# Performance work log

Measured on AMD Instinct MI355X. Metric: run time of the kernel, lower is better.

Reference implementation:

```python
import jax, jax.numpy as jnp
import numpy as np

B, T, D = 8, 1024, 256
H, KD = 8, 256          # keras MHA built with key_dim=embed_dim -> per-head dim = D
FF = 1024
WIN = 64                # causal sliding window size
G = 2                   # num_global_tokens (last-k tokens of the sequence)
EPS = 1e-6
NEG = -1e9


def _mha(q_in, kv_in, Wq, bq, Wk, bk, Wv, bv, Wo, bo, mask=None):
    """Keras-style MultiHeadAttention. q_in:[B,Tq,D], kv_in:[B,Ts,D] -> [B,Tq,D]."""
    q = jnp.einsum('btd,dhk->bthk', q_in, Wq) + bq
    k = jnp.einsum('bsd,dhk->bshk', kv_in, Wk) + bk
    v = jnp.einsum('bsd,dhk->bshk', kv_in, Wv) + bv
    s = jnp.einsum('bthk,bshk->bhts', q, k) / jnp.sqrt(jnp.asarray(KD, q.dtype))
    if mask is not None:
        s = jnp.where(mask, s, jnp.asarray(NEG, s.dtype))
    a = jax.nn.softmax(s, axis=-1)
    o = jnp.einsum('bhts,bshk->bthk', a, v)
    return jnp.einsum('bthk,hkd->btd', o, Wo) + bo


def _ln(x, g, b):
    m = jnp.mean(x, axis=-1, keepdims=True)
    v = jnp.mean(jnp.square(x - m), axis=-1, keepdims=True)
    return (x - m) * jax.lax.rsqrt(v + EPS) * g + b


def setup_inputs() -> dict:
    key = jax.random.key(0)
    ks = jax.random.split(key, 32)
    sp = 1.0 / np.sqrt(D)   # proj fan-in D
    so = 1.0 / np.sqrt(H * KD)

    def mha_params(k0):
        k = jax.random.split(k0, 4)
        return dict(
            Wq=jax.random.normal(k[0], (D, H, KD), jnp.float32) * sp,
            Wk=jax.random.normal(k[1], (D, H, KD), jnp.float32) * sp,
            Wv=jax.random.normal(k[2], (D, H, KD), jnp.float32) * sp,
            Wo=jax.random.normal(k[3], (H, KD, D), jnp.float32) * so,
        )
    lp = mha_params(ks[1])
    gp = mha_params(ks[2])
    inp = {
        'x': jax.random.normal(ks[0], (B, T, D), jnp.float32),
        'lWq': lp['Wq'], 'lbq': jnp.zeros((H, KD), jnp.float32),
        'lWk': lp['Wk'], 'lbk': jnp.zeros((H, KD), jnp.float32),
        'lWv': lp['Wv'], 'lbv': jnp.zeros((H, KD), jnp.float32),
        'lWo': lp['Wo'], 'lbo': jnp.zeros((D,), jnp.float32),
        'gWq': gp['Wq'], 'gbq': jnp.zeros((H, KD), jnp.float32),
        'gWk': gp['Wk'], 'gbk': jnp.zeros((H, KD), jnp.float32),
        'gWv': gp['Wv'], 'gbv': jnp.zeros((H, KD), jnp.float32),
        'gWo': gp['Wo'], 'gbo': jnp.zeros((D,), jnp.float32),
        'fW1': jax.random.normal(ks[3], (D, FF), jnp.float32) * sp,
        'fb1': jnp.zeros((FF,), jnp.float32),
        'fW2': jax.random.normal(ks[4], (FF, D), jnp.float32) * (1.0 / np.sqrt(FF)),
        'fb2': jnp.zeros((D,), jnp.float32),
        'ln1_g': jnp.ones((D,), jnp.float32), 'ln1_b': jnp.zeros((D,), jnp.float32),
        'ln2_g': jnp.ones((D,), jnp.float32), 'ln2_b': jnp.zeros((D,), jnp.float32),
    }
    return inp


def reference(x, lWq, lbq, lWk, lbk, lWv, lbv, lWo, lbo,
              gWq, gbq, gWk, gbk, gWv, gbv, gWo, gbo,
              fW1, fb1, fW2, fb2, ln1_g, ln1_b, ln2_g, ln2_b):
    i = jnp.arange(T)[:, None]
    j = jnp.arange(T)[None, :]
    win_mask = (j <= i) & (j > i - WIN)            # [T,T]
    win_mask = win_mask[None, None]                # [1,1,T,T]

    # Local window attention (the original per-timestep loop, fused via mask).
    local = _mha(x, x, lWq, lbq, lWk, lbk, lWv, lbv, lWo, lbo, mask=win_mask)

    # Global tokens: last G tokens attend to full sequence, then tokens attend to them.
    g = x[:, T - G:, :]                            # [B,G,D]
    g2 = _mha(g, x, gWq, gbq, gWk, gbk, gWv, gbv, gWo, gbo)
    gx = _mha(x, g2, gWq, gbq, gWk, gbk, gWv, gbv, gWo, gbo)

    attn_out = local + gx
    out1 = _ln(x + attn_out, ln1_g, ln1_b)
    ffn = jnp.maximum(out1 @ fW1 + fb1, 0.0) @ fW2 + fb2
    return _ln(out1 + ffn, ln2_g, ln2_b)
```

## Files before the change

kernel.cpp:

```cpp
#include <hip/hip_runtime.h>
#include <hip/hip_bf16.h>

#define B_ 8
#define T_ 1024
#define D_ 256
#define H_ 8
#define KD_ 256
#define HK_ 2048
#define FF_ 1024
#define WIN_ 64
#define BT_ 8192
#define SX_ 10240

using bf16 = __hip_bfloat16;
typedef float f32x4 __attribute__((ext_vector_type(4)));
typedef short s16x8 __attribute__((ext_vector_type(8)));

__device__ inline float b2f(bf16 h) { return __bfloat162float(h); }
__device__ inline float bs2f(short s) {
    unsigned int u = ((unsigned int)(unsigned short)s) << 16;
    return __builtin_bit_cast(float, u);
}
__device__ inline float us2f(unsigned short s) {
    unsigned int u = ((unsigned int)s) << 16;
    return __builtin_bit_cast(float, u);
}
__device__ inline unsigned short fbits(float x) { bf16 h = __float2bfloat16(x); return __builtin_bit_cast(unsigned short, h); }

__device__ __forceinline__ void stage16(const void* g, void* l) {
    __builtin_amdgcn_global_load_lds((const __attribute__((address_space(1))) void*)g,
                                     (__attribute__((address_space(3))) void*)l, 16, 0, 0);
}

__global__ __launch_bounds__(256) void f32_to_bf16_vec(const float* __restrict__ in, bf16* __restrict__ out, int n) {
    int i = (blockIdx.x * 256 + threadIdx.x) * 4;
    if (i + 3 < n) {
        float4 v = *(const float4*)(in + i);
        ushort4 o;
        o.x = fbits(v.x); o.y = fbits(v.y); o.z = fbits(v.z); o.w = fbits(v.w);
        *(ushort4*)(out + i) = o;
    }
}

struct TJob { const float* in; bf16* out; int R; int C; int os; int tile_start; };
struct TJobs { TJob j[10]; int total; };

__global__ void transpose_all(TJobs js) {
    __shared__ float tile[32][33];
    int bid = blockIdx.x;
    int ji = 0;
    while (ji < 9 && bid >= js.j[ji + 1].tile_start) ji++;
    TJob jb = js.j[ji];
    int t = bid - jb.tile_start;
    int tiles_x = jb.C / 32;
    int cb = (t % tiles_x) * 32, rb = (t / tiles_x) * 32;
    for (int k = 0; k < 4; k++) {
        int r = threadIdx.y + k * 8;
        tile[r][threadIdx.x] = jb.in[(size_t)(rb + r) * jb.C + cb + threadIdx.x];
    }
    __syncthreads();
    for (int k = 0; k < 4; k++) {
        int r = threadIdx.y + k * 8;
        jb.out[(size_t)(cb + r) * jb.os + rb + threadIdx.x] = __float2bfloat16(tile[threadIdx.x][r]);
    }
}

__global__ __launch_bounds__(256) void concat_bias10(const float* a0, const float* a1, const float* a2,
                                                     const float* a3, const float* a4, float* out) {
    int i = blockIdx.x * 256 + threadIdx.x;
    int seg = i >> 11, off = i & 2047;
    const float* p = seg == 0 ? a0 : seg == 1 ? a1 : seg == 2 ? a2 : seg == 3 ? a3 : a4;
    out[i] = p[off];
}

template <int MODE, int BN>
__global__ __launch_bounds__(256) void gemm128(const bf16* __restrict__ A, const bf16* __restrict__ Bt,
                                               const float* __restrict__ bias, bf16* __restrict__ C,
                                               int M, int N, int K) {
    constexpr int NF = BN / 32;
    constexpr int ABUF = 128 * 64;
    constexpr int BBUF = BN * 64;
    constexpr int BUFE = ABUF + BBUF;
    constexpr int EC = BN + 8;
    constexpr int ARENA_E = (2 * BUFE > 128 * EC) ? 2 * BUFE : 128 * EC;
    __shared__ __align__(16) bf16 arena[ARENA_E];
    const int tid = threadIdx.x;
    const int w = tid >> 6, l = tid & 63;
    const int m0 = blockIdx.y * 128, n0 = blockIdx.x * BN;
    const int wm = (w >> 1) * 64, wn = (w & 1) * (BN / 2);
    const int srow = w * 8 + (l >> 3);
    const int scol = ((l & 7) ^ (l >> 3)) * 8;
    const int ldsOff = w * 512;
    const int nt = K / 64;

    auto stageT = [&](int buf, int k0) {
        bf16* Ad = arena + buf * BUFE;
        bf16* Bd = Ad + ABUF;
#pragma unroll
        for (int j = 0; j < 4; j++)
            stage16(A + (size_t)(m0 + j * 32 + srow) * K + k0 + scol, &Ad[ldsOff + j * 2048]);
#pragma unroll
        for (int j = 0; j < NF; j++)
            stage16(Bt + (size_t)(n0 + j * 32 + srow) * K + k0 + scol, &Bd[ldsOff + j * 2048]);
    };

    f32x4 acc[4][NF] = {};
    stageT(0, 0);
    __syncthreads();
    int cur = 0;
    for (int t = 0; t < nt; t++) {
        if (t + 1 < nt) stageT(cur ^ 1, (t + 1) * 64);
        const bf16* As = arena + cur * BUFE;
        const bf16* Bs = As + ABUF;
#pragma unroll
        for (int ks = 0; ks < 2; ks++) {
            s16x8 a[4], b[NF];
#pragma unroll
            for (int mf = 0; mf < 4; mf++) {
                int ar = wm + mf * 16 + (l & 15);
                int ch = (ks * 4 + (l >> 4)) ^ (ar & 7);
                a[mf] = *(const s16x8*)&As[ar * 64 + ch * 8];
            }
#pragma unroll
            for (int nf = 0; nf < NF; nf++) {
                int br = wn + nf * 16 + (l & 15);
                int ch = (ks * 4 + (l >> 4)) ^ (br & 7);
                b[nf] = *(const s16x8*)&Bs[br * 64 + ch * 8];
            }
            __builtin_amdgcn_s_setprio(1);
#pragma unroll
            for (int mf = 0; mf < 4; mf++)
#pragma unroll
                for (int nf = 0; nf < NF; nf++)
                    acc[mf][nf] = __builtin_amdgcn_mfma_f32_16x16x32_bf16(a[mf], b[nf], acc[mf][nf], 0, 0, 0);
            __builtin_amdgcn_s_setprio(0);
        }
        __syncthreads();
        cur ^= 1;
    }
    bf16* Es = arena;
#pragma unroll
    for (int mf = 0; mf < 4; mf++)
#pragma unroll
        for (int nf = 0; nf < NF; nf++)
#pragma unroll
            for (int r = 0; r < 4; r++) {
                int row = wm + mf * 16 + (l >> 4) * 4 + r;
                int col = wn + nf * 16 + (l & 15);
                float v = acc[mf][nf][r] + bias[n0 + col];
                if (MODE == 2) v = fmaxf(v, 0.f);
                Es[row * EC + col] = __float2bfloat16(v);
            }
    __syncthreads();
    constexpr int RPC = BN / 8;
    constexpr int CPT = (128 * BN) / (256 * 8);
#pragma unroll
    for (int c = 0; c < CPT; c++) {
        int lin = c * 256 + tid;
        int row = lin / RPC, cc = lin - row * RPC;
        s16x8 v = *(const s16x8*)&Es[row * EC + cc * 8];
        *(s16x8*)(C + (size_t)(m0 + row) * N + n0 + cc * 8) = v;
    }
}

__global__ __launch_bounds__(256) void local_attn(const bf16* __restrict__ XW, bf16* __restrict__ O) {
    __shared__ bf16 U[256 * 72];
    __shared__ bf16 Ps[64][136];
    const int tid = threadIdx.x, l = tid & 63, w = tid >> 6;
    const int qt = blockIdx.x, bh = blockIdx.y;
    const int b = bh >> 3, h = bh & 7;
    const int qs = qt * 64;
    const int r0 = w * 16;
    const int lrow = tid >> 2, lc4 = (tid & 3) * 8;
    const size_t obase = (size_t)b * T_ * HK_ + h * KD_;

    s16x8 qa[8];
    {
        const bf16* qbase = XW + (size_t)(b * T_ + qs + r0 + (l & 15)) * SX_ + h * KD_ + (l >> 4) * 8;
#pragma unroll
        for (int ks = 0; ks < 8; ks++) qa[ks] = *(const s16x8*)(qbase + ks * 32);
    }

    bf16(*Ks)[264] = (bf16(*)[264])U;
    {
        int tk = qs - 64 + lrow;
        const bf16* krow = XW + (size_t)(b * T_ + tk) * SX_ + 2048 + h * KD_;
#pragma unroll
        for (int c = 0; c < 8; c++) {
            int col = lc4 + c * 32;
            uint4 val = {0, 0, 0, 0};
            if (tk >= 0) val = *(const uint4*)(krow + col);
            *(uint4*)&Ks[lrow][col] = val;
        }
    }
    __syncthreads();
    f32x4 sacc[8];
#pragma unroll
    for (int f = 0; f < 8; f++) sacc[f] = (f32x4){0.f, 0.f, 0.f, 0.f};
    __builtin_amdgcn_s_setprio(1);
#pragma unroll
    for (int nf = 0; nf < 4; nf++)
#pragma unroll
        for (int ks = 0; ks < 8; ks++) {
            s16x8 bb = *(const s16x8*)&Ks[nf * 16 + (l & 15)][ks * 32 + (l >> 4) * 8];
            sacc[nf] = __builtin_amdgcn_mfma_f32_16x16x32_bf16(qa[ks], bb, sacc[nf], 0, 0, 0);
        }
    __builtin_amdgcn_s_setprio(0);
    __syncthreads();
    {
        const bf16* krow = XW + (size_t)(b * T_ + qs + lrow) * SX_ + 2048 + h * KD_;
#pragma unroll
        for (int c = 0; c < 8; c++) {
            int col = lc4 + c * 32;
            *(uint4*)&Ks[lrow][col] = *(const uint4*)(krow + col);
        }
    }
    __syncthreads();
    __builtin_amdgcn_s_setprio(1);
#pragma unroll
    for (int nf = 0; nf < 4; nf++)
#pragma unroll
        for (int ks = 0; ks < 8; ks++) {
            s16x8 bb = *(const s16x8*)&Ks[nf * 16 + (l & 15)][ks * 32 + (l >> 4) * 8];
            sacc[4 + nf] = __builtin_amdgcn_mfma_f32_16x16x32_bf16(qa[ks], bb, sacc[4 + nf], 0, 0, 0);
        }
    __builtin_amdgcn_s_setprio(0);

    uint4 vreg[8];
    {
        int tk = qs - 64 + lrow;
        const bf16* vrow = XW + (size_t)(b * T_ + tk) * SX_ + 4096 + h * KD_;
#pragma unroll
        for (int c = 0; c < 8; c++) {
            uint4 v = {0, 0, 0, 0};
            if (tk >= 0) v = *(const uint4*)(vrow + lc4 + c * 32);
            vreg[c] = v;
        }
    }

#pragma unroll
    for (int r = 0; r < 4; r++) {
        int i = qs + r0 + (l >> 4) * 4 + r;
#pragma unroll
        for (int f = 0; f < 8; f++) {
            int j = qs - 64 + f * 16 + (l & 15);
            bool valid = (j >= 0) && (j <= i) && (j > i - WIN_);
            sacc[f][r] = valid ? sacc[f][r] * (1.f / 16.f) : -1e9f;
        }
        float mm = -1e30f;
#pragma unroll
        for (int f = 0; f < 8; f++) mm = fmaxf(mm, sacc[f][r]);
        mm = fmaxf(mm, __shfl_xor(mm, 1, 64));
        mm = fmaxf(mm, __shfl_xor(mm, 2, 64));
        mm = fmaxf(mm, __shfl_xor(mm, 4, 64));
        mm = fmaxf(mm, __shfl_xor(mm, 8, 64));
        float ss = 0.f;
#pragma unroll
        for (int f = 0; f < 8; f++) {
            float e = __expf(sacc[f][r] - mm);
            sacc[f][r] = e;
            ss += e;
        }
        ss += __shfl_xor(ss, 1, 64);
        ss += __shfl_xor(ss, 2, 64);
        ss += __shfl_xor(ss, 4, 64);
        ss += __shfl_xor(ss, 8, 64);
        float inv = 1.f / ss;
#pragma unroll
        for (int f = 0; f < 8; f++) sacc[f][r] *= inv;
    }
    __syncthreads();

    bf16(*VT)[72] = (bf16(*)[72])U;
#pragma unroll
    for (int f = 0; f < 8; f++)
#pragma unroll
        for (int r = 0; r < 4; r++)
            Ps[r0 + (l >> 4) * 4 + r][f * 16 + (l & 15)] = __float2bfloat16(sacc[f][r]);
#pragma unroll
    for (int c = 0; c < 8; c++) {
        int col = lc4 + c * 32;
        bf16 tmp[8];
        *(uint4*)tmp = vreg[c];
        for (int e = 0; e < 8; e++) VT[col + e][lrow] = tmp[e];
    }
    __syncthreads();
    {
        const bf16* vrow = XW + (size_t)(b * T_ + qs + lrow) * SX_ + 4096 + h * KD_;
#pragma unroll
        for (int c = 0; c < 8; c++) vreg[c] = *(const uint4*)(vrow + lc4 + c * 32);
    }

    f32x4 oacc[16];
#pragma unroll
    for (int nf = 0; nf < 16; nf++) oacc[nf] = (f32x4){0.f, 0.f, 0.f, 0.f};
    for (int kb = 0; kb < 2; kb++) {
#pragma unroll
        for (int ks = 0; ks < 2; ks++) {
            s16x8 a = *(const s16x8*)&Ps[r0 + (l & 15)][kb * 64 + ks * 32 + (l >> 4) * 8];
            __builtin_amdgcn_s_setprio(1);
#pragma unroll
            for (int nf = 0; nf < 16; nf++) {
                s16x8 bb = *(const s16x8*)&VT[nf * 16 + (l & 15)][ks * 32 + (l >> 4) * 8];
                oacc[nf] = __builtin_amdgcn_mfma_f32_16x16x32_bf16(a, bb, oacc[nf], 0, 0, 0);
            }
            __builtin_amdgcn_s_setprio(0);
        }
        if (kb == 0) {
            __syncthreads();
#pragma unroll
            for (int c = 0; c < 8; c++) {
                int col = lc4 + c * 32;
                bf16 tmp[8];
                *(uint4*)tmp = vreg[c];
                for (int e = 0; e < 8; e++) VT[col + e][lrow] = tmp[e];
            }
            __syncthreads();
        }
    }
#pragma unroll
    for (int nf = 0; nf < 16; nf++)
#pragma unroll
        for (int r = 0; r < 4; r++) {
            int row = r0 + (l >> 4) * 4 + r;
            int col = nf * 16 + (l & 15);
            O[obase + (size_t)(qs + row) * HK_ + col] = __float2bfloat16(oacc[nf][r]);
        }
}

__global__ __launch_bounds__(256) void qg_kernel(const float* __restrict__ x, const bf16* __restrict__ gwq_t,
                                                 const float* __restrict__ gbq, float* __restrict__ qg) {
    __shared__ float xs[256];
    int bi = blockIdx.x, ch = blockIdx.y, tid = threadIdx.x;
    int b = bi >> 1, i = bi & 1;
    xs[tid] = x[((size_t)b * T_ + (T_ - 2 + i)) * D_ + tid];
    __syncthreads();
    int hk = ch * 256 + tid;
    const bf16* wr = gwq_t + (size_t)hk * D_;
    float acc = gbq[hk];
    for (int c = 0; c < 32; c++) {
        s16x8 wv = *(const s16x8*)&wr[c * 8];
#pragma unroll
        for (int e = 0; e < 8; e++) acc += xs[c * 8 + e] * bs2f(wv[e]);
    }
    qg[(size_t)bi * HK_ + hk] = acc;
}

__global__ __launch_bounds__(256) void g2_scores(const float* __restrict__ qg, const bf16* __restrict__ XW,
                                                 float* __restrict__ sc) {
    __shared__ float qf[2][256];
    int bh = blockIdx.x, ch = blockIdx.y;
    int b = bh >> 3, h = bh & 7;
    int tid = threadIdx.x;
    for (int i = 0; i < 2; i++)
        qf[i][tid] = qg[(size_t)(b * 2 + i) * HK_ + h * KD_ + tid];
    __syncthreads();
    int t = ch * 256 + tid;
    const bf16* kr = &XW[((size_t)(b * T_ + t)) * SX_ + 6144 + h * KD_];
    float a0 = 0.f, a1 = 0.f;
    for (int c = 0; c < 32; c++) {
        s16x8 kv = *(const s16x8*)&kr[c * 8];
#pragma unroll
        for (int e = 0; e < 8; e++) {
            float kf = bs2f(kv[e]);
            a0 += kf * qf[0][c * 8 + e];
            a1 += kf * qf[1][c * 8 + e];
        }
    }
    sc[((size_t)bh * 2 + 0) * T_ + t] = a0 * (1.f / 16.f);
    sc[((size_t)bh * 2 + 1) * T_ + t] = a1 * (1.f / 16.f);
}

__global__ __launch_bounds__(256) void g2_softmax(float* __restrict__ sc) {
    __shared__ float red[4];
    int bh = blockIdx.x, tid = threadIdx.x;
    int w = tid >> 6;
    for (int i = 0; i < 2; i++) {
        float* row = &sc[((size_t)bh * 2 + i) * T_];
        float vals[4];
        float m = -1e30f;
        for (int c = 0; c < 4; c++) {
            vals[c] = row[tid + 256 * c];
            m = fmaxf(m, vals[c]);
        }
        for (int s = 32; s >= 1; s >>= 1) m = fmaxf(m, __shfl_xor(m, s, 64));
        if ((tid & 63) == 0) red[w] = m;
        __syncthreads();
        m = fmaxf(fmaxf(red[0], red[1]), fmaxf(red[2], red[3]));
        __syncthreads();
        float s = 0.f;
        for (int c = 0; c < 4; c++) {
            vals[c] = __expf(vals[c] - m);
            s += vals[c];
        }
        for (int d = 32; d >= 1; d >>= 1) s += __shfl_xor(s, d, 64);
        if ((tid & 63) == 0) red[w] = s;
        __syncthreads();
        s = red[0] + red[1] + red[2] + red[3];
        float inv = 1.f / s;
        for (int c = 0; c < 4; c++) row[tid + 256 * c] = vals[c] * inv;
        __syncthreads();
    }
}

__global__ __launch_bounds__(256) void g2_pv(const float* __restrict__ sc, const bf16* __restrict__ XW,
                                             float* __restrict__ og_part) {
    __shared__ float p2[2][256];
    int bh = blockIdx.x, ch = blockIdx.y;
    int b = bh >> 3, h = bh & 7;
    int tid = threadIdx.x;
    for (int i = 0; i < 2; i++) p2[i][tid] = sc[((size_t)bh * 2 + i) * T_ + ch * 256 + tid];
    __syncthreads();
    const bf16* vb = &XW[((size_t)(b * T_ + ch * 256)) * SX_ + 8192 + h * KD_ + tid];
    float a0 = 0.f, a1 = 0.f;
    for (int t = 0; t < 256; t++) {
        float vv = b2f(vb[(size_t)t * SX_]);
        a0 += p2[0][t] * vv;
        a1 += p2[1][t] * vv;
    }
    og_part[((size_t)(bh * 4 + ch) * 2 + 0) * KD_ + tid] = a0;
    og_part[((size_t)(bh * 4 + ch) * 2 + 1) * KD_ + tid] = a1;
}

__global__ __launch_bounds__(256) void g2_lin2(const float* __restrict__ og_part, const bf16* __restrict__ gwoT,
                                               const float* __restrict__ gbo, float* __restrict__ g2buf) {
    __shared__ float og_row[2048];
    int bi = blockIdx.x, tid = threadIdx.x;
    int b = bi >> 1, i = bi & 1;
#pragma unroll
    for (int j = 0; j < 8; j++) {
        int idx = j * 256 + tid;
        int h = idx >> 8, kd = idx & 255;
        int bh = b * 8 + h;
        float s = 0.f;
#pragma unroll
        for (int ch = 0; ch < 4; ch++)
            s += og_part[((size_t)(bh * 4 + ch) * 2 + i) * KD_ + kd];
        og_row[idx] = s;
    }
    __syncthreads();
    int d = blockIdx.y * 16 + (tid >> 4);
    int s16i = tid & 15;
    const float* ogr = og_row + s16i * 128;
    const bf16* wr = gwoT + (size_t)d * HK_ + s16i * 128;
    float acc = 0.f;
    for (int c = 0; c < 16; c++) {
        s16x8 wv = *(const s16x8*)&wr[c * 8];
#pragma unroll
        for (int e = 0; e < 8; e++) acc += ogr[c * 8 + e] * bs2f(wv[e]);
    }
    acc += __shfl_xor(acc, 1, 64);
    acc += __shfl_xor(acc, 2, 64);
    acc += __shfl_xor(acc, 4, 64);
    acc += __shfl_xor(acc, 8, 64);
    if (s16i == 0) g2buf[(size_t)bi * 256 + d] = acc + gbo[d];
}

__global__ __launch_bounds__(256) void g2_kva2(const float* __restrict__ g2buf, const bf16* __restrict__ gwk_t,
                                               const float* __restrict__ gbk, const bf16* __restrict__ gwv_t,
                                               const float* __restrict__ gbv, const bf16* __restrict__ gwq_t,
                                               const bf16* __restrict__ gwoT, const float* __restrict__ gbq,
                                               float* __restrict__ A2, float* __restrict__ W2,
                                               float* __restrict__ c2) {
    __shared__ float g2s[256], k2s[256], v2s[256];
    __shared__ float red[4];
    int bi = blockIdx.x, h = blockIdx.y, tid = threadIdx.x;
    g2s[tid] = g2buf[(size_t)bi * 256 + tid];
    __syncthreads();
    int hk = h * 256 + tid;
    {
        const bf16* rk = &gwk_t[(size_t)hk * D_];
        const bf16* rv = &gwv_t[(size_t)hk * D_];
        float ak = gbk[hk], av = gbv[hk];
        for (int c = 0; c < 32; c++) {
            s16x8 kw = *(const s16x8*)&rk[c * 8];
            s16x8 vw = *(const s16x8*)&rv[c * 8];
#pragma unroll
            for (int e = 0; e < 8; e++) {
                float g = g2s[c * 8 + e];
                ak += g * bs2f(kw[e]);
                av += g * bs2f(vw[e]);
            }
        }
        k2s[tid] = ak;
        v2s[tid] = av;
    }
    __syncthreads();
    float accA = 0.f;
    const bf16* wq = gwq_t + (size_t)(h * 256) * D_ + tid;
    for (int kd = 0; kd < 256; kd++)
        accA += k2s[kd] * b2f(wq[(size_t)kd * D_]);
    float accW = 0.f;
    const bf16* wo = gwoT + (size_t)tid * HK_ + h * 256;
    for (int c = 0; c < 32; c++) {
        s16x8 wv = *(const s16x8*)&wo[c * 8];
#pragma unroll
        for (int e = 0; e < 8; e++) accW += v2s[c * 8 + e] * bs2f(wv[e]);
    }
    int o = (bi * 8 + h) * 256 + tid;
    A2[o] = accA;
    W2[o] = accW;
    float pc = gbq[h * 256 + tid] * k2s[tid];
#pragma unroll
    for (int m = 32; m >= 1; m >>= 1) pc += __shfl_xor(pc, m, 64);
    if ((tid & 63) == 0) red[tid >> 6] = pc;
    __syncthreads();
    if (tid == 0) c2[bi * 8 + h] = red[0] + red[1] + red[2] + red[3];
}

__global__ __launch_bounds__(256) void ln1_gx(const float* __restrict__ x, const bf16* __restrict__ attnL,
                                              const float* __restrict__ A2, const float* __restrict__ W2,
                                              const float* __restrict__ c2, const float* __restrict__ gbo,
                                              const float* __restrict__ g, const float* __restrict__ bia,
                                              bf16* __restrict__ outb) {
    int w = threadIdx.x >> 6, l = threadIdx.x & 63;
    int t = blockIdx.x * 4 + w;
    int b = t >> 10;
    size_t base = (size_t)t * D_ + l * 4;
    float4 x4 = *(const float4*)(x + base);
    float p[8][2];
#pragma unroll
    for (int h = 0; h < 8; h++)
#pragma unroll
        for (int i = 0; i < 2; i++) {
            float4 a4 = *(const float4*)(A2 + ((size_t)((b * 2 + i) * 8 + h)) * 256 + l * 4);
            float dt = x4.x * a4.x + x4.y * a4.y + x4.z * a4.z + x4.w * a4.w;
#pragma unroll
            for (int m = 32; m >= 1; m >>= 1) dt += __shfl_xor(dt, m, 64);
            p[h][i] = dt;
        }
    float4 gb = *(const float4*)(gbo + l * 4);
    float o0 = gb.x, o1 = gb.y, o2 = gb.z, o3 = gb.w;
#pragma unroll
    for (int h = 0; h < 8; h++) {
        float s0 = (p[h][0] + c2[(b * 2 + 0) * 8 + h]) * (1.f / 16.f);
        float s1 = (p[h][1] + c2[(b * 2 + 1) * 8 + h]) * (1.f / 16.f);
        float mx = fmaxf(s0, s1);
        float e0 = __expf(s0 - mx), e1 = __expf(s1 - mx);
        float inv = 1.f / (e0 + e1);
        float p0 = e0 * inv, p1 = e1 * inv;
        float4 w0 = *(const float4*)(W2 + ((size_t)((b * 2 + 0) * 8 + h)) * 256 + l * 4);
        float4 w1 = *(const float4*)(W2 + ((size_t)((b * 2 + 1) * 8 + h)) * 256 + l * 4);
        o0 += p0 * w0.x + p1 * w1.x;
        o1 += p0 * w0.y + p1 * w1.y;
        o2 += p0 * w0.z + p1 * w1.z;
        o3 += p0 * w0.w + p1 * w1.w;
    }
    ushort4 av = *(const ushort4*)((const unsigned short*)attnL + base);
    float vv[4];
    vv[0] = x4.x + us2f(av.x) + o0;
    vv[1] = x4.y + us2f(av.y) + o1;
    vv[2] = x4.z + us2f(av.z) + o2;
    vv[3] = x4.w + us2f(av.w) + o3;
    float s = vv[0] + vv[1] + vv[2] + vv[3];
#pragma unroll
    for (int m = 32; m >= 1; m >>= 1) s += __shfl_xor(s, m, 64);
    float mean = s * (1.f / 256.f);
    float q = 0.f;
#pragma unroll
    for (int e = 0; e < 4; e++) {
        float d = vv[e] - mean;
        q += d * d;
    }
#pragma unroll
    for (int m = 32; m >= 1; m >>= 1) q += __shfl_xor(q, m, 64);
    float rs = rsqrtf(q * (1.f / 256.f) + 1e-6f);
    float4 gv = *(const float4*)(g + l * 4);
    float4 biv = *(const float4*)(bia + l * 4);
    ushort4 ou;
    ou.x = fbits((vv[0] - mean) * rs * gv.x + biv.x);
    ou.y = fbits((vv[1] - mean) * rs * gv.y + biv.y);
    ou.z = fbits((vv[2] - mean) * rs * gv.z + biv.z);
    ou.w = fbits((vv[3] - mean) * rs * gv.w + biv.w);
    *(ushort4*)((unsigned short*)outb + base) = ou;
}

template <typename TA, bool HASC>
__global__ __launch_bounds__(256) void ln_kernel(const TA* __restrict__ a, const bf16* __restrict__ b2,
                                                 const bf16* __restrict__ c, const float* __restrict__ g,
                                                 const float* __restrict__ bia, float* __restrict__ outf,
                                                 bf16* __restrict__ outb) {
    int w = threadIdx.x >> 6, l = threadIdx.x & 63;
    int row = blockIdx.x * 4 + w;
    size_t base = (size_t)row * D_ + l * 4;
    float vv[4];
    if constexpr (sizeof(TA) == 4) {
        float4 av = *(const float4*)((const float*)a + base);
        vv[0] = av.x; vv[1] = av.y; vv[2] = av.z; vv[3] = av.w;
    } else {
        ushort4 av = *(const ushort4*)((const unsigned short*)a + base);
        vv[0] = us2f(av.x); vv[1] = us2f(av.y); vv[2] = us2f(av.z); vv[3] = us2f(av.w);
    }
    ushort4 bv = *(const ushort4*)((const unsigned short*)b2 + base);
    vv[0] += us2f(bv.x); vv[1] += us2f(bv.y); vv[2] += us2f(bv.z); vv[3] += us2f(bv.w);
    if constexpr (HASC) {
        ushort4 cv = *(const ushort4*)((const unsigned short*)c + base);
        vv[0] += us2f(cv.x); vv[1] += us2f(cv.y); vv[2] += us2f(cv.z); vv[3] += us2f(cv.w);
    }
    float s = vv[0] + vv[1] + vv[2] + vv[3];
#pragma unroll
    for (int m = 32; m >= 1; m >>= 1) s += __shfl_xor(s, m, 64);
    float mean = s * (1.f / 256.f);
    float q = 0.f;
#pragma unroll
    for (int e = 0; e < 4; e++) {
        float d = vv[e] - mean;
        q += d * d;
    }
#pragma unroll
    for (int m = 32; m >= 1; m >>= 1) q += __shfl_xor(q, m, 64);
    float rs = rsqrtf(q * (1.f / 256.f) + 1e-6f);
    float4 gv = *(const float4*)(g + l * 4);
    float4 biv = *(const float4*)(bia + l * 4);
    float o0 = (vv[0] - mean) * rs * gv.x + biv.x;
    float o1 = (vv[1] - mean) * rs * gv.y + biv.y;
    float o2 = (vv[2] - mean) * rs * gv.z + biv.z;
    float o3 = (vv[3] - mean) * rs * gv.w + biv.w;
    if (outf) *(float4*)(outf + base) = (float4){o0, o1, o2, o3};
    if (outb) {
        ushort4 ou;
        ou.x = fbits(o0); ou.y = fbits(o1); ou.z = fbits(o2); ou.w = fbits(o3);
        *(ushort4*)(outb + base) = ou;
    }
}

extern "C" void kernel_launch(void* const* d_in, const int* in_sizes, int n_in, void* d_out, int out_size,
                              void* d_ws, size_t ws_size, hipStream_t stream) {
    const float* x = (const float*)d_in[0];
    const float* lWq = (const float*)d_in[1];  const float* lbq = (const float*)d_in[2];
    const float* lWk = (const float*)d_in[3];  const float* lbk = (const float*)d_in[4];
    const float* lWv = (const float*)d_in[5];  const float* lbv = (const float*)d_in[6];
    const float* lWo = (const float*)d_in[7];  const float* lbo = (const float*)d_in[8];
    const float* gWq = (const float*)d_in[9];  const float* gbq = (const float*)d_in[10];
    const float* gWk = (const float*)d_in[11]; const float* gbk = (const float*)d_in[12];
    const float* gWv = (const float*)d_in[13]; const float* gbv = (const float*)d_in[14];
    const float* gWo = (const float*)d_in[15]; const float* gbo = (const float*)d_in[16];
    const float* fW1 = (const float*)d_in[17]; const float* fb1 = (const float*)d_in[18];
    const float* fW2 = (const float*)d_in[19]; const float* fb2 = (const float*)d_in[20];
    const float* ln1g = (const float*)d_in[21]; const float* ln1b = (const float*)d_in[22];
    const float* ln2g = (const float*)d_in[23]; const float* ln2b = (const float*)d_in[24];

    char* ws = (char*)d_ws;
    size_t off = 0;
    auto alloc = [&](size_t bytes) -> char* {
        char* p = ws + off;
        off = (off + bytes + 255) & ~(size_t)255;
        return p;
    };
    bf16* xb = (bf16*)alloc((size_t)BT_ * D_ * 2);
    bf16* W10 = (bf16*)alloc((size_t)SX_ * D_ * 2);
    bf16* gwq_t = (bf16*)alloc((size_t)HK_ * D_ * 2);
    bf16* woL = (bf16*)alloc((size_t)D_ * HK_ * 2);
    bf16* gwoT = (bf16*)alloc((size_t)D_ * HK_ * 2);
    bf16* fw1_t = (bf16*)alloc((size_t)FF_ * D_ * 2);
    bf16* fw2_t = (bf16*)alloc((size_t)D_ * FF_ * 2);
    float* bcat10 = (float*)alloc((size_t)SX_ * 4);
    bf16* XW = (bf16*)alloc((size_t)BT_ * SX_ * 2);
    bf16* Ob = (bf16*)alloc((size_t)BT_ * HK_ * 2);
    bf16* attnL = (bf16*)alloc((size_t)BT_ * D_ * 2);
    float* sc = (float*)alloc((size_t)B_ * H_ * 2 * T_ * 4);
    float* og_part = (float*)alloc((size_t)B_ * H_ * 4 * 2 * KD_ * 4);
    float* g2buf = (float*)alloc((size_t)B_ * 2 * D_ * 4);
    float* qg = (float*)alloc((size_t)B_ * 2 * HK_ * 4);
    float* A2 = (float*)alloc((size_t)16 * 8 * 256 * 4);
    float* W2 = (float*)alloc((size_t)16 * 8 * 256 * 4);
    float* c2 = (float*)alloc((size_t)16 * 8 * 4);
    bf16* hid = XW;
    bf16* ffn = (bf16*)((char*)XW + (32u << 20));
    bf16* out1b = (bf16*)((char*)XW + (48u << 20));

    f32_to_bf16_vec<<<(BT_ * D_) / 1024, 256, 0, stream>>>(x, xb, BT_ * D_);
    {
        TJobs js;
        int t = 0;
        auto add = [&](int i, const float* in, bf16* out, int R, int C, int os) {
            js.j[i] = {in, out, R, C, os, t};
            t += (R / 32) * (C / 32);
        };
        add(0, lWq, W10, D_, HK_, D_);
        add(1, lWk, W10 + (size_t)2048 * D_, D_, HK_, D_);
        add(2, lWv, W10 + (size_t)4096 * D_, D_, HK_, D_);
        add(3, gWk, W10 + (size_t)6144 * D_, D_, HK_, D_);
        add(4, gWv, W10 + (size_t)8192 * D_, D_, HK_, D_);
        add(5, gWq, gwq_t, D_, HK_, D_);
        add(6, lWo, woL, HK_, D_, HK_);
        add(7, gWo, gwoT, HK_, D_, HK_);
        add(8, fW1, fw1_t, D_, FF_, D_);
        add(9, fW2, fw2_t, FF_, D_, FF_);
        js.total = t;
        transpose_all<<<t, dim3(32, 8), 0, stream>>>(js);
    }
    concat_bias10<<<SX_ / 256, 256, 0, stream>>>(lbq, lbk, lbv, gbk, gbv, bcat10);
    qg_kernel<<<dim3(16, 8), 256, 0, stream>>>(x, gwq_t, gbq, qg);

    gemm128<1, 128><<<dim3(SX_ / 128, BT_ / 128), 256, 0, stream>>>(xb, W10, bcat10, XW, BT_, SX_, D_);

    local_attn<<<dim3(T_ / 64, B_ * H_), 256, 0, stream>>>(XW, Ob);
    gemm128<1, 64><<<dim3(D_ / 64, BT_ / 128), 256, 0, stream>>>(Ob, woL, lbo, attnL, BT_, D_, HK_);

    g2_scores<<<dim3(B_ * H_, T_ / 256), 256, 0, stream>>>(qg, XW, sc);
    g2_softmax<<<B_ * H_, 256, 0, stream>>>(sc);
    g2_pv<<<dim3(B_ * H_, 4), 256, 0, stream>>>(sc, XW, og_part);
    g2_lin2<<<dim3(B_ * 2, 16), 256, 0, stream>>>(og_part, gwoT, gbo, g2buf);
    g2_kva2<<<dim3(16, 8), 256, 0, stream>>>(g2buf, W10 + (size_t)6144 * D_, gbk,
                                             W10 + (size_t)8192 * D_, gbv, gwq_t, gwoT, gbq, A2, W2, c2);

    ln1_gx<<<BT_ / 4, 256, 0, stream>>>(x, attnL, A2, W2, c2, gbo, ln1g, ln1b, out1b);
    gemm128<2, 128><<<dim3(FF_ / 128, BT_ / 128), 256, 0, stream>>>(out1b, fw1_t, fb1, hid, BT_, FF_, D_);
    gemm128<1, 64><<<dim3(D_ / 64, BT_ / 128), 256, 0, stream>>>(hid, fw2_t, fb2, ffn, BT_, D_, FF_);
    ln_kernel<bf16, false><<<BT_ / 4, 256, 0, stream>>>(out1b, ffn, nullptr, ln2g, ln2b, (float*)d_out, nullptr);
}
```

Measured before the change: 260.4 us.

## Reassociate global-token attention to skip projecting global K/V for every token

The global-token branch no longer projects K and V for all 8192 tokens. Scores are computed as x·(Wk q) plus a bias term, and the attention-weighted sum is taken over raw x before applying Wv. This shrinks the big QKV GEMM from 10240 to 6144 output columns and cuts the XW buffer, and the f32-to-bf16 conversion is fused into the new score kernel. The cost is several small extra kernels, fp32 reductions over x, and slightly different rounding in the global path.

```diff
diff --git a/kernel.cpp b/kernel.cpp
--- a/kernel.cpp
+++ b/kernel.cpp
@@ -10,7 +10,7 @@
 #define FF_ 1024
 #define WIN_ 64
 #define BT_ 8192
-#define SX_ 10240
+#define S6_ 6144
 
 using bf16 = __hip_bfloat16;
 typedef float f32x4 __attribute__((ext_vector_type(4)));
@@ -30,16 +30,6 @@
 __device__ __forceinline__ void stage16(const void* g, void* l) {
     __builtin_amdgcn_global_load_lds((const __attribute__((address_space(1))) void*)g,
                                      (__attribute__((address_space(3))) void*)l, 16, 0, 0);
-}
-
-__global__ __launch_bounds__(256) void f32_to_bf16_vec(const float* __restrict__ in, bf16* __restrict__ out, int n) {
-    int i = (blockIdx.x * 256 + threadIdx.x) * 4;
-    if (i + 3 < n) {
-        float4 v = *(const float4*)(in + i);
-        ushort4 o;
-        o.x = fbits(v.x); o.y = fbits(v.y); o.z = fbits(v.z); o.w = fbits(v.w);
-        *(ushort4*)(out + i) = o;
-    }
 }
 
 struct TJob { const float* in; bf16* out; int R; int C; int os; int tile_start; };
@@ -65,12 +55,11 @@
     }
 }
 
-__global__ __launch_bounds__(256) void concat_bias10(const float* a0, const float* a1, const float* a2,
-                                                     const float* a3, const float* a4, float* out) {
+__global__ __launch_bounds__(256) void concat_bias6(const float* a0, const float* a1, const float* a2,
+                                                    float* out) {
     int i = blockIdx.x * 256 + threadIdx.x;
     int seg = i >> 11, off = i & 2047;
-    const float* p = seg == 0 ? a0 : seg == 1 ? a1 : seg == 2 ? a2 : seg == 3 ? a3 : a4;
-    out[i] = p[off];
+    out[i] = (seg == 0 ? a0 : seg == 1 ? a1 : a2)[off];
 }
 
 template <int MODE, int BN>
@@ -176,7 +165,7 @@
 
     s16x8 qa[8];
     {
-        const bf16* qbase = XW + (size_t)(b * T_ + qs + r0 + (l & 15)) * SX_ + h * KD_ + (l >> 4) * 8;
+        const bf16* qbase = XW + (size_t)(b * T_ + qs + r0 + (l & 15)) * S6_ + h * KD_ + (l >> 4) * 8;
 #pragma unroll
         for (int ks = 0; ks < 8; ks++) qa[ks] = *(const s16x8*)(qbase + ks * 32);
     }
@@ -184,7 +173,7 @@
     bf16(*Ks)[264] = (bf16(*)[264])U;
     {
         int tk = qs - 64 + lrow;
-        const bf16* krow = XW + (size_t)(b * T_ + tk) * SX_ + 2048 + h * KD_;
+        const bf16* krow = XW + (size_t)(b * T_ + tk) * S6_ + 2048 + h * KD_;
 #pragma unroll
         for (int c = 0; c < 8; c++) {
             int col = lc4 + c * 32;
@@ -208,7 +197,7 @@
     __builtin_amdgcn_s_setprio(0);
     __syncthreads();
     {
-        const bf16* krow = XW + (size_t)(b * T_ + qs + lrow) * SX_ + 2048 + h * KD_;
+        const bf16* krow = XW + (size_t)(b * T_ + qs + lrow) * S6_ + 2048 + h * KD_;
 #pragma unroll
         for (int c = 0; c < 8; c++) {
             int col = lc4 + c * 32;
@@ -229,7 +218,7 @@
     uint4 vreg[8];
     {
         int tk = qs - 64 + lrow;
-        const bf16* vrow = XW + (size_t)(b * T_ + tk) * SX_ + 4096 + h * KD_;
+        const bf16* vrow = XW + (size_t)(b * T_ + tk) * S6_ + 4096 + h * KD_;
 #pragma unroll
         for (int c = 0; c < 8; c++) {
             uint4 v = {0, 0, 0, 0};
@@ -286,7 +275,7 @@
     }
     __syncthreads();
     {
-        const bf16* vrow = XW + (size_t)(b * T_ + qs + lrow) * SX_ + 4096 + h * KD_;
+        const bf16* vrow = XW + (size_t)(b * T_ + qs + lrow) * S6_ + 4096 + h * KD_;
 #pragma unroll
         for (int c = 0; c < 8; c++) vreg[c] = *(const uint4*)(vrow + lc4 + c * 32);
     }
@@ -346,29 +335,48 @@
     qg[(size_t)bi * HK_ + hk] = acc;
 }
 
-__global__ __launch_bounds__(256) void g2_scores(const float* __restrict__ qg, const bf16* __restrict__ XW,
-                                                 float* __restrict__ sc) {
-    __shared__ float qf[2][256];
-    int bh = blockIdx.x, ch = blockIdx.y;
-    int b = bh >> 3, h = bh & 7;
-    int tid = threadIdx.x;
-    for (int i = 0; i < 2; i++)
-        qf[i][tid] = qg[(size_t)(b * 2 + i) * HK_ + h * KD_ + tid];
-    __syncthreads();
-    int t = ch * 256 + tid;
-    const bf16* kr = &XW[((size_t)(b * T_ + t)) * SX_ + 6144 + h * KD_];
-    float a0 = 0.f, a1 = 0.f;
-    for (int c = 0; c < 32; c++) {
-        s16x8 kv = *(const s16x8*)&kr[c * 8];
-#pragma unroll
-        for (int e = 0; e < 8; e++) {
-            float kf = bs2f(kv[e]);
-            a0 += kf * qf[0][c * 8 + e];
-            a1 += kf * qf[1][c * 8 + e];
-        }
-    }
-    sc[((size_t)bh * 2 + 0) * T_ + t] = a0 * (1.f / 16.f);
-    sc[((size_t)bh * 2 + 1) * T_ + t] = a1 * (1.f / 16.f);
+__global__ __launch_bounds__(256) void qk_kernel(const float* __restrict__ qg, const bf16* __restrict__ gwk_t,
+                                                 const float* __restrict__ gbk, float* __restrict__ qk,
+                                                 float* __restrict__ cb) {
+    __shared__ float qgs[256];
+    __shared__ float red[4];
+    int bi = blockIdx.x, h = blockIdx.y, tid = threadIdx.x;
+    qgs[tid] = qg[(size_t)bi * HK_ + h * 256 + tid];
+    __syncthreads();
+    float acc = 0.f;
+    const bf16* wcol = gwk_t + (size_t)(h * 256) * D_ + tid;
+    for (int kd = 0; kd < 256; kd++) acc += qgs[kd] * b2f(wcol[(size_t)kd * D_]);
+    qk[(size_t)(bi * 8 + h) * 256 + tid] = acc;
+    float pc = qgs[tid] * gbk[h * 256 + tid];
+#pragma unroll
+    for (int m = 32; m >= 1; m >>= 1) pc += __shfl_xor(pc, m, 64);
+    if ((tid & 63) == 0) red[tid >> 6] = pc;
+    __syncthreads();
+    if (tid == 0) cb[bi * 8 + h] = red[0] + red[1] + red[2] + red[3];
+}
+
+__global__ __launch_bounds__(256) void conv_scores(const float* __restrict__ x, bf16* __restrict__ xb,
+                                                   const float* __restrict__ qk, const float* __restrict__ cb,
+                                                   float* __restrict__ sc) {
+    int w = threadIdx.x >> 6, l = threadIdx.x & 63;
+    int t = blockIdx.x * 4 + w;
+    int b = t >> 10, tl = t & 1023;
+    size_t base = (size_t)t * D_ + l * 4;
+    float4 x4 = *(const float4*)(x + base);
+    ushort4 o;
+    o.x = fbits(x4.x); o.y = fbits(x4.y); o.z = fbits(x4.z); o.w = fbits(x4.w);
+    *(ushort4*)((unsigned short*)xb + base) = o;
+#pragma unroll
+    for (int h = 0; h < 8; h++)
+#pragma unroll
+        for (int i = 0; i < 2; i++) {
+            int bi = b * 2 + i;
+            float4 a4 = *(const float4*)(qk + (size_t)(bi * 8 + h) * 256 + l * 4);
+            float dt = x4.x * a4.x + x4.y * a4.y + x4.z * a4.z + x4.w * a4.w;
+#pragma unroll
+            for (int m = 32; m >= 1; m >>= 1) dt += __shfl_xor(dt, m, 64);
+            if (l == 0) sc[((size_t)((b * 8 + h) * 2 + i)) * T_ + tl] = (dt + cb[bi * 8 + h]) * (1.f / 16.f);
+        }
 }
 
 __global__ __launch_bounds__(256) void g2_softmax(float* __restrict__ sc) {
@@ -403,45 +411,53 @@
     }
 }
 
-__global__ __launch_bounds__(256) void g2_pv(const float* __restrict__ sc, const bf16* __restrict__ XW,
-                                             float* __restrict__ og_part) {
+__global__ __launch_bounds__(256) void xbar_kernel(const float* __restrict__ sc, const float* __restrict__ x,
+                                                   float* __restrict__ xbar_part) {
     __shared__ float p2[2][256];
     int bh = blockIdx.x, ch = blockIdx.y;
-    int b = bh >> 3, h = bh & 7;
+    int b = bh >> 3;
     int tid = threadIdx.x;
     for (int i = 0; i < 2; i++) p2[i][tid] = sc[((size_t)bh * 2 + i) * T_ + ch * 256 + tid];
     __syncthreads();
-    const bf16* vb = &XW[((size_t)(b * T_ + ch * 256)) * SX_ + 8192 + h * KD_ + tid];
+    const float* xp = x + ((size_t)(b * T_ + ch * 256)) * D_ + tid;
     float a0 = 0.f, a1 = 0.f;
     for (int t = 0; t < 256; t++) {
-        float vv = b2f(vb[(size_t)t * SX_]);
-        a0 += p2[0][t] * vv;
-        a1 += p2[1][t] * vv;
-    }
-    og_part[((size_t)(bh * 4 + ch) * 2 + 0) * KD_ + tid] = a0;
-    og_part[((size_t)(bh * 4 + ch) * 2 + 1) * KD_ + tid] = a1;
-}
-
-__global__ __launch_bounds__(256) void g2_lin2(const float* __restrict__ og_part, const bf16* __restrict__ gwoT,
+        float xv = xp[(size_t)t * D_];
+        a0 += p2[0][t] * xv;
+        a1 += p2[1][t] * xv;
+    }
+    xbar_part[((size_t)(bh * 4 + ch) * 2 + 0) * KD_ + tid] = a0;
+    xbar_part[((size_t)(bh * 4 + ch) * 2 + 1) * KD_ + tid] = a1;
+}
+
+__global__ __launch_bounds__(256) void g2_vo(const float* __restrict__ xbar_part, const bf16* __restrict__ gwv_t,
+                                             const float* __restrict__ gbv, float* __restrict__ og2) {
+    __shared__ float xbs[256];
+    int bi = blockIdx.x, h = blockIdx.y, tid = threadIdx.x;
+    int b = bi >> 1, i = bi & 1;
+    int bh = b * 8 + h;
+    float s = 0.f;
+#pragma unroll
+    for (int ch = 0; ch < 4; ch++) s += xbar_part[((size_t)(bh * 4 + ch) * 2 + i) * KD_ + tid];
+    xbs[tid] = s;
+    __syncthreads();
+    int hk = h * 256 + tid;
+    const bf16* wr = gwv_t + (size_t)hk * D_;
+    float acc = gbv[hk];
+    for (int c = 0; c < 32; c++) {
+        s16x8 wv = *(const s16x8*)&wr[c * 8];
+#pragma unroll
+        for (int e = 0; e < 8; e++) acc += xbs[c * 8 + e] * bs2f(wv[e]);
+    }
+    og2[(size_t)bi * HK_ + hk] = acc;
+}
+
+__global__ __launch_bounds__(256) void g2_lin2(const float* __restrict__ og2, const bf16* __restrict__ gwoT,
                                                const float* __restrict__ gbo, float* __restrict__ g2buf) {
-    __shared__ float og_row[2048];
     int bi = blockIdx.x, tid = threadIdx.x;
-    int b = bi >> 1, i = bi & 1;
-#pragma unroll
-    for (int j = 0; j < 8; j++) {
-        int idx = j * 256 + tid;
-        int h = idx >> 8, kd = idx & 255;
-        int bh = b * 8 + h;
-        float s = 0.f;
-#pragma unroll
-        for (int ch = 0; ch < 4; ch++)
-            s += og_part[((size_t)(bh * 4 + ch) * 2 + i) * KD_ + kd];
-        og_row[idx] = s;
-    }
-    __syncthreads();
     int d = blockIdx.y * 16 + (tid >> 4);
     int s16i = tid & 15;
-    const float* ogr = og_row + s16i * 128;
+    const float* ogr = og2 + (size_t)bi * 2048 + s16i * 128;
     const bf16* wr = gwoT + (size_t)d * HK_ + s16i * 128;
     float acc = 0.f;
     for (int c = 0; c < 16; c++) {
@@ -648,20 +664,25 @@
         return p;
     };
     bf16* xb = (bf16*)alloc((size_t)BT_ * D_ * 2);
-    bf16* W10 = (bf16*)alloc((size_t)SX_ * D_ * 2);
+    bf16* W6 = (bf16*)alloc((size_t)S6_ * D_ * 2);
     bf16* gwq_t = (bf16*)alloc((size_t)HK_ * D_ * 2);
+    bf16* gwk_t = (bf16*)alloc((size_t)HK_ * D_ * 2);
+    bf16* gwv_t = (bf16*)alloc((size_t)HK_ * D_ * 2);
     bf16* woL = (bf16*)alloc((size_t)D_ * HK_ * 2);
     bf16* gwoT = (bf16*)alloc((size_t)D_ * HK_ * 2);
     bf16* fw1_t = (bf16*)alloc((size_t)FF_ * D_ * 2);
     bf16* fw2_t = (bf16*)alloc((size_t)D_ * FF_ * 2);
-    float* bcat10 = (float*)alloc((size_t)SX_ * 4);
-    bf16* XW = (bf16*)alloc((size_t)BT_ * SX_ * 2);
+    float* bcat6 = (float*)alloc((size_t)S6_ * 4);
+    bf16* XW = (bf16*)alloc((size_t)BT_ * S6_ * 2);
     bf16* Ob = (bf16*)alloc((size_t)BT_ * HK_ * 2);
     bf16* attnL = (bf16*)alloc((size_t)BT_ * D_ * 2);
     float* sc = (float*)alloc((size_t)B_ * H_ * 2 * T_ * 4);
-    float* og_part = (float*)alloc((size_t)B_ * H_ * 4 * 2 * KD_ * 4);
+    float* xbar_part = (float*)alloc((size_t)B_ * H_ * 4 * 2 * KD_ * 4);
+    float* og2 = (float*)alloc((size_t)16 * HK_ * 4);
     float* g2buf = (float*)alloc((size_t)B_ * 2 * D_ * 4);
     float* qg = (float*)alloc((size_t)B_ * 2 * HK_ * 4);
+    float* qk = (float*)alloc((size_t)16 * 8 * 256 * 4);
+    float* cb = (float*)alloc((size_t)16 * 8 * 4);
     float* A2 = (float*)alloc((size_t)16 * 8 * 256 * 4);
     float* W2 = (float*)alloc((size_t)16 * 8 * 256 * 4);
     float* c2 = (float*)alloc((size_t)16 * 8 * 4);
@@ -669,7 +690,6 @@
     bf16* ffn = (bf16*)((char*)XW + (32u << 20));
     bf16* out1b = (bf16*)((char*)XW + (48u << 20));
 
-    f32_to_bf16_vec<<<(BT_ * D_) / 1024, 256, 0, stream>>>(x, xb, BT_ * D_);
     {
         TJobs js;
         int t = 0;
@@ -677,12 +697,12 @@
             js.j[i] = {in, out, R, C, os, t};
             t += (R / 32) * (C / 32);
         };
-        add(0, lWq, W10, D_, HK_, D_);
-        add(1, lWk, W10 + (size_t)2048 * D_, D_, HK_, D_);
-        add(2, lWv, W10 + (size_t)4096 * D_, D_, HK_, D_);
-        add(3, gWk, W10 + (size_t)6144 * D_, D_, HK_, D_);
-        add(4, gWv, W10 + (size_t)8192 * D_, D_, HK_, D_);
-        add(5, gWq, gwq_t, D_, HK_, D_);
+        add(0, lWq, W6, D_, HK_, D_);
+        add(1, lWk, W6 + (size_t)2048 * D_, D_, HK_, D_);
+        add(2, lWv, W6 + (size_t)4096 * D_, D_, HK_, D_);
+        add(3, gWq, gwq_t, D_, HK_, D_);
+        add(4, gWk, gwk_t, D_, HK_, D_);
+        add(5, gWv, gwv_t, D_, HK_, D_);
         add(6, lWo, woL, HK_, D_, HK_);
         add(7, gWo, gwoT, HK_, D_, HK_);
         add(8, fW1, fw1_t, D_, FF_, D_);
@@ -690,20 +710,22 @@
         js.total = t;
         transpose_all<<<t, dim3(32, 8), 0, stream>>>(js);
     }
-    concat_bias10<<<SX_ / 256, 256, 0, stream>>>(lbq, lbk, lbv, gbk, gbv, bcat10);
+    concat_bias6<<<S6_ / 256, 256, 0, stream>>>(lbq, lbk, lbv, bcat6);
     qg_kernel<<<dim3(16, 8), 256, 0, stream>>>(x, gwq_t, gbq, qg);
-
-    gemm128<1, 128><<<dim3(SX_ / 128, BT_ / 128), 256, 0, stream>>>(xb, W10, bcat10, XW, BT_, SX_, D_);
+    qk_kernel<<<dim3(16, 8), 256, 0, stream>>>(qg, gwk_t, gbk, qk, cb);
+
+    conv_scores<<<BT_ / 4, 256, 0, stream>>>(x, xb, qk, cb, sc);
+
+    gemm128<1, 128><<<dim3(S6_ / 128, BT_ / 128), 256, 0, stream>>>(xb, W6, bcat6, XW, BT_, S6_, D_);
 
     local_attn<<<dim3(T_ / 64, B_ * H_), 256, 0, stream>>>(XW, Ob);
     gemm128<1, 64><<<dim3(D_ / 64, BT_ / 128), 256, 0, stream>>>(Ob, woL, lbo, attnL, BT_, D_, HK_);
 
-    g2_scores<<<dim3(B_ * H_, T_ / 256), 256, 0, stream>>>(qg, XW, sc);
     g2_softmax<<<B_ * H_, 256, 0, stream>>>(sc);
-    g2_pv<<<dim3(B_ * H_, 4), 256, 0, stream>>>(sc, XW, og_part);
-    g2_lin2<<<dim3(B_ * 2, 16), 256, 0, stream>>>(og_part, gwoT, gbo, g2buf);
-    g2_kva2<<<dim3(16, 8), 256, 0, stream>>>(g2buf, W10 + (size_t)6144 * D_, gbk,
-                                             W10 + (size_t)8192 * D_, gbv, gwq_t, gwoT, gbq, A2, W2, c2);
+    xbar_kernel<<<dim3(B_ * H_, 4), 256, 0, stream>>>(sc, x, xbar_part);
+    g2_vo<<<dim3(16, 8), 256, 0, stream>>>(xbar_part, gwv_t, gbv, og2);
+    g2_lin2<<<dim3(16, 16), 256, 0, stream>>>(og2, gwoT, gbo, g2buf);
+    g2_kva2<<<dim3(16, 8), 256, 0, stream>>>(g2buf, gwk_t, gbk, gwv_t, gbv, gwq_t, gwoT, gbq, A2, W2, c2);
 
     ln1_gx<<<BT_ / 4, 256, 0, stream>>>(x, attnL, A2, W2, c2, gbo, ln1g, ln1b, out1b);
     gemm128<2, 128><<<dim3(FF_ / 128, BT_ / 128), 256, 0, stream>>>(out1b, fw1_t, fb1, hid, BT_, FF_, D_);
```

After: 240.3 us, median of 2. -7.7%, faster.
